# Kernel optimization log

Measured on AMD Instinct MI355X. Metric: run time of the kernel, lower is better.

The kernel has to match this reference:

```python
import jax, jax.numpy as jnp
import numpy as np

N_QUBITS = 4
N_LAYERS = 2
BN_EPS = 1e-5


def _bcast(t, ref):
    t = jnp.asarray(t)
    return t.reshape(t.shape + (1,) * (ref.ndim - t.ndim))


def apply_ry(state, theta, wire):
    # state: [B, 2,2,2,2] complex; theta: scalar or [B]
    ax = wire + 1
    s0 = jnp.take(state, 0, axis=ax)
    s1 = jnp.take(state, 1, axis=ax)
    half = jnp.asarray(theta, jnp.float32) * 0.5
    c = _bcast(jnp.cos(half), s0)
    s = _bcast(jnp.sin(half), s0)
    return jnp.stack([c * s0 - s * s1, s * s0 + c * s1], axis=ax)


def apply_rz(state, theta, wire):
    ax = wire + 1
    s0 = jnp.take(state, 0, axis=ax)
    s1 = jnp.take(state, 1, axis=ax)
    half = jnp.asarray(theta, jnp.float32) * 0.5
    p = _bcast(jnp.exp(-1j * half), s0)  # complex64
    return jnp.stack([p * s0, jnp.conj(p) * s1], axis=ax)


def apply_cnot(state, control, target):
    ca, ta = control + 1, target + 1
    c0 = jnp.take(state, 0, axis=ca)
    c1 = jnp.take(state, 1, axis=ca)
    ta2 = ta - 1 if ta > ca else ta  # axis shift after take
    c1 = jnp.flip(c1, axis=ta2)      # X on target within control=1 block
    return jnp.stack([c0, c1], axis=ca)


def quantum_layer(x_q_in, qw):
    # Faithful to QuantumLayer.forward: extra tanh on (already tanh'd) input.
    B = x_q_in.shape[0]
    ang = jnp.tanh(x_q_in) * jnp.float32(np.pi)  # [B, n_qubits]
    state = jnp.zeros((B, 2 ** N_QUBITS), jnp.complex64).at[:, 0].set(1.0)
    state = state.reshape((B,) + (2,) * N_QUBITS)
    for i in range(N_QUBITS):
        state = apply_ry(state, ang[:, i], i)
    for l in range(N_LAYERS):
        for i in range(N_QUBITS):
            state = apply_ry(state, qw[l, i, 0], i)
            state = apply_rz(state, qw[l, i, 1], i)
        for i in range(N_QUBITS):
            state = apply_cnot(state, i, (i + 1) % N_QUBITS)
    probs = state.real ** 2 + state.imag ** 2  # [B,2,2,2,2]
    zs = []
    for i in range(N_QUBITS):
        d = jnp.take(probs, 0, axis=i + 1) - jnp.take(probs, 1, axis=i + 1)
        zs.append(jnp.sum(d, axis=tuple(range(1, d.ndim))))
    return jnp.stack(zs, axis=1).astype(jnp.float32)  # [B, n_qubits]


def forward(x, W1, b1, bn_g, bn_b, bn_m, bn_v, W2, b2, qw, W3, b3):
    # pre_quantum (eval mode: dropouts are identity)
    h = jax.nn.relu(x @ W1.T + b1)                       # [B,64]
    h = (h - bn_m) * jax.lax.rsqrt(bn_v + BN_EPS) * bn_g + bn_b
    xq = jnp.tanh(h @ W2.T + b2)                          # [B,4]
    q = quantum_layer(xq, qw)                             # [B,4]
    return q @ W3.T + b3                                  # [B,num_classes]


def setup_inputs() -> dict:
    key = jax.random.key(0)
    ks = jax.random.split(key, 8)
    B, D, H, Q, C = 32768, 1280, 64, N_QUBITS, 10
    return {
        "x": jax.random.normal(ks[0], (B, D), jnp.float32),
        "W1": jax.random.normal(ks[1], (H, D), jnp.float32) * 0.02,
        "b1": jnp.zeros((H,), jnp.float32),
        "bn_g": jnp.ones((H,), jnp.float32),
        "bn_b": jnp.zeros((H,), jnp.float32),
        "bn_m": jnp.zeros((H,), jnp.float32),
        "bn_v": jnp.ones((H,), jnp.float32),
        "W2": jax.random.normal(ks[2], (Q, H), jnp.float32) * 0.1,
        "b2": jnp.zeros((Q,), jnp.float32),
        "qw": jax.random.normal(ks[3], (N_LAYERS, Q, 2), jnp.float32) * 0.1,
        "W3": jax.random.normal(ks[4], (C, Q), jnp.float32) * 0.1,
        "b3": jnp.zeros((C,), jnp.float32),
    }


def reference(x, W1, b1, bn_g, bn_b, bn_m, bn_v, W2, b2, qw, W3, b3):
    return forward(x, W1, b1, bn_g, bn_b, bn_m, bn_v, W2, b2, qw, W3, b3)
```

## Files before the change

kernel.cpp:

```cpp
#include <hip/hip_runtime.h>
#include <math.h>

typedef __attribute__((ext_vector_type(8))) short bf16x8;
typedef __attribute__((ext_vector_type(4))) float f32x4;

constexpr int D   = 1280;
constexpr int H   = 64;
constexpr int BM  = 64;
constexpr int KC  = 64;
constexpr int SW  = KC + 8;
constexpr int HSS = H + 1;

union FragU { bf16x8 v; unsigned int u[4]; };

__device__ __forceinline__ unsigned int pack_split(float f0, float f1, unsigned int& lo) {
    unsigned int u0 = __float_as_uint(f0), u1 = __float_as_uint(f1);
    unsigned int h0 = u0 & 0xFFFF0000u,    h1 = u1 & 0xFFFF0000u;
    float l0 = f0 - __uint_as_float(h0);
    float l1 = f1 - __uint_as_float(h1);
    lo = (__float_as_uint(l1) & 0xFFFF0000u) | (__float_as_uint(l0) >> 16);
    return h1 | (u0 >> 16);
}

template<int BW>
__device__ __forceinline__ void ry_gate(float re[16], float im[16], float theta) {
    float sn, cs;
    sincosf(0.5f * theta, &sn, &cs);
#pragma unroll
    for (int s0 = 0; s0 < 16; ++s0) {
        if (s0 & BW) continue;
        const int s1 = s0 | BW;
        float r0 = re[s0], i0 = im[s0], r1 = re[s1], i1 = im[s1];
        re[s0] = cs * r0 - sn * r1;  im[s0] = cs * i0 - sn * i1;
        re[s1] = sn * r0 + cs * r1;  im[s1] = sn * i0 + cs * i1;
    }
}

template<int BW>
__device__ __forceinline__ void rz_gate(float re[16], float im[16], float theta) {
    float sn, cs;
    sincosf(0.5f * theta, &sn, &cs);
#pragma unroll
    for (int s0 = 0; s0 < 16; ++s0) {
        if (s0 & BW) continue;
        const int s1 = s0 | BW;
        float r0 = re[s0], i0 = im[s0], r1 = re[s1], i1 = im[s1];
        re[s0] = cs * r0 + sn * i0;  im[s0] = cs * i0 - sn * r0;
        re[s1] = cs * r1 - sn * i1;  im[s1] = cs * i1 + sn * r1;
    }
}

template<int BWC, int BWT>
__device__ __forceinline__ void cnot_gate(float re[16], float im[16]) {
#pragma unroll
    for (int s = 0; s < 16; ++s) {
        if (!(s & BWC)) continue;
        if (s & BWT) continue;
        const int t = s | BWT;
        float tr = re[s], ti = im[s];
        re[s] = re[t]; im[s] = im[t];
        re[t] = tr;    im[t] = ti;
    }
}

__global__ __launch_bounds__(256, 2)
void fused_qh_mfma(const float* __restrict__ x,   const float* __restrict__ W1,
                   const float* __restrict__ b1,  const float* __restrict__ bn_g,
                   const float* __restrict__ bn_b,const float* __restrict__ bn_m,
                   const float* __restrict__ bn_v,const float* __restrict__ W2,
                   const float* __restrict__ b2,  const float* __restrict__ qw,
                   const float* __restrict__ W3,  const float* __restrict__ b3,
                   float* __restrict__ out)
{
    __shared__ short whi[H][SW];
    __shared__ short wlo[H][SW];
    __shared__ float hs[BM][HSS];
    __shared__ float w2s[4 * H];
    __shared__ float b1s[H], scl[H], shf[H];

    const int tid  = threadIdx.x;
    const int l    = tid & 63;
    const int w    = tid >> 6;
    const int lr   = l & 15;
    const int lk   = l >> 4;
    const int row0 = blockIdx.x * BM;

    w2s[tid] = W2[tid];
    if (tid < H) {
        float s = bn_g[tid] * rsqrtf(bn_v[tid] + 1e-5f);
        b1s[tid] = b1[tid];
        scl[tid] = s;
        shf[tid] = bn_b[tid] - bn_m[tid] * s;
    }

    const float4* xr4 = reinterpret_cast<const float4*>(x + (size_t)(row0 + w * 16 + lr) * D);

    int sn[4], sk4[4];
#pragma unroll
    for (int it = 0; it < 4; ++it) {
        int f4 = tid + it * 256;
        sn[it]  = f4 >> 4;
        sk4[it] = (f4 & 15) * 4;
    }

    f32x4 acc[4] = {{0,0,0,0},{0,0,0,0},{0,0,0,0},{0,0,0,0}};

    float4 acur[4], anxt[4], wcur[4], wnxt[4];
#pragma unroll
    for (int it = 0; it < 4; ++it)
        wcur[it] = *reinterpret_cast<const float4*>(&W1[(size_t)sn[it] * D + sk4[it]]);
#pragma unroll
    for (int h = 0; h < 2; ++h)
#pragma unroll
        for (int p = 0; p < 2; ++p)
            acur[h * 2 + p] = xr4[h * 8 + lk * 2 + p];

    for (int k0 = 0; k0 < D; k0 += KC) {
#pragma unroll
        for (int it = 0; it < 4; ++it) {
            unsigned int lo01, lo23;
            unsigned int hi01 = pack_split(wcur[it].x, wcur[it].y, lo01);
            unsigned int hi23 = pack_split(wcur[it].z, wcur[it].w, lo23);
            uint2 hv; hv.x = hi01; hv.y = hi23;
            uint2 lv; lv.x = lo01; lv.y = lo23;
            *reinterpret_cast<uint2*>(&whi[sn[it]][sk4[it]]) = hv;
            *reinterpret_cast<uint2*>(&wlo[sn[it]][sk4[it]]) = lv;
        }
        if (k0 + KC < D) {
            const int kn = k0 + KC;
#pragma unroll
            for (int it = 0; it < 4; ++it)
                wnxt[it] = *reinterpret_cast<const float4*>(&W1[(size_t)sn[it] * D + kn + sk4[it]]);
#pragma unroll
            for (int h = 0; h < 2; ++h)
#pragma unroll
                for (int p = 0; p < 2; ++p)
                    anxt[h * 2 + p] = xr4[kn / 4 + h * 8 + lk * 2 + p];
        }
        __syncthreads();

        FragU ahi[2], alo[2];
#pragma unroll
        for (int h = 0; h < 2; ++h) {
            const float4 a0 = acur[h * 2 + 0];
            const float4 a1 = acur[h * 2 + 1];
            ahi[h].u[0] = pack_split(a0.x, a0.y, alo[h].u[0]);
            ahi[h].u[1] = pack_split(a0.z, a0.w, alo[h].u[1]);
            ahi[h].u[2] = pack_split(a1.x, a1.y, alo[h].u[2]);
            ahi[h].u[3] = pack_split(a1.z, a1.w, alo[h].u[3]);
        }

#pragma unroll
        for (int h = 0; h < 2; ++h) {
#pragma unroll
            for (int g = 0; g < 4; ++g) {
                const bf16x8 bh = *reinterpret_cast<const bf16x8*>(&whi[g * 16 + lr][h * 32 + lk * 8]);
                const bf16x8 bl = *reinterpret_cast<const bf16x8*>(&wlo[g * 16 + lr][h * 32 + lk * 8]);
                acc[g] = __builtin_amdgcn_mfma_f32_16x16x32_bf16(ahi[h].v, bh, acc[g], 0, 0, 0);
                acc[g] = __builtin_amdgcn_mfma_f32_16x16x32_bf16(ahi[h].v, bl, acc[g], 0, 0, 0);
                acc[g] = __builtin_amdgcn_mfma_f32_16x16x32_bf16(alo[h].v, bh, acc[g], 0, 0, 0);
            }
        }
        __syncthreads();

#pragma unroll
        for (int it = 0; it < 4; ++it) { acur[it] = anxt[it]; wcur[it] = wnxt[it]; }
    }

#pragma unroll
    for (int g = 0; g < 4; ++g) {
        const int c = g * 16 + lr;
        const float b1c = b1s[c], s = scl[c], sh = shf[c];
#pragma unroll
        for (int r = 0; r < 4; ++r) {
            float v = acc[g][r] + b1c;
            v = fmaxf(v, 0.0f) * s + sh;
            hs[w * 16 + lk * 4 + r][c] = v;
        }
    }
    __syncthreads();

    if (tid < BM) {
        const int row = tid;

        float ang[4];
#pragma unroll
        for (int qi = 0; qi < 4; ++qi) {
            float a2 = b2[qi];
            for (int k = 0; k < H; ++k)
                a2 = fmaf(hs[row][k], w2s[qi * H + k], a2);
            float xq = tanhf(a2);
            ang[qi] = tanhf(xq) * 3.14159265358979323846f;
        }

        float re[16] = {}, im[16] = {};
        re[0] = 1.0f;
        ry_gate<8>(re, im, ang[0]);
        ry_gate<4>(re, im, ang[1]);
        ry_gate<2>(re, im, ang[2]);
        ry_gate<1>(re, im, ang[3]);

#pragma unroll
        for (int ll = 0; ll < 2; ++ll) {
            const float* qp = &qw[ll * 8];
            ry_gate<8>(re, im, qp[0]); rz_gate<8>(re, im, qp[1]);
            ry_gate<4>(re, im, qp[2]); rz_gate<4>(re, im, qp[3]);
            ry_gate<2>(re, im, qp[4]); rz_gate<2>(re, im, qp[5]);
            ry_gate<1>(re, im, qp[6]); rz_gate<1>(re, im, qp[7]);
            cnot_gate<8, 4>(re, im);
            cnot_gate<4, 2>(re, im);
            cnot_gate<2, 1>(re, im);
            cnot_gate<1, 8>(re, im);
        }

        float z[4] = {};
#pragma unroll
        for (int s = 0; s < 16; ++s) {
            float p = re[s] * re[s] + im[s] * im[s];
            z[0] += (s & 8) ? -p : p;
            z[1] += (s & 4) ? -p : p;
            z[2] += (s & 2) ? -p : p;
            z[3] += (s & 1) ? -p : p;
        }

        float* o = &out[(size_t)(row0 + row) * 10];
#pragma unroll
        for (int c = 0; c < 10; ++c) {
            float v = b3[c];
#pragma unroll
            for (int i = 0; i < 4; ++i)
                v = fmaf(z[i], W3[c * 4 + i], v);
            o[c] = v;
        }
    }
}

extern "C" void kernel_launch(void* const* d_in, const int* in_sizes, int n_in,
                              void* d_out, int out_size, void* d_ws, size_t ws_size,
                              hipStream_t stream) {
    const float* x    = (const float*)d_in[0];
    const float* W1   = (const float*)d_in[1];
    const float* b1   = (const float*)d_in[2];
    const float* bn_g = (const float*)d_in[3];
    const float* bn_b = (const float*)d_in[4];
    const float* bn_m = (const float*)d_in[5];
    const float* bn_v = (const float*)d_in[6];
    const float* W2   = (const float*)d_in[7];
    const float* b2   = (const float*)d_in[8];
    const float* qw   = (const float*)d_in[9];
    const float* W3   = (const float*)d_in[10];
    const float* b3   = (const float*)d_in[11];
    float* out = (float*)d_out;

    const int B = in_sizes[0] / D;
    const int grid = B / BM;

    fused_qh_mfma<<<grid, 256, 0, stream>>>(
        x, W1, b1, bn_g, bn_b, bn_m, bn_v, W2, b2, qw, W3, b3, out);
}
```

Measured before the change: 43.69 us.

## Pre-split W1 into MFMA fragment layout in workspace and drop LDS staging

Adds a pre-pass kernel that splits W1 into bf16 hi/lo parts, stored in MFMA fragment order in the workspace. The main kernel then reads B fragments straight from global memory (L2-resident), with no LDS tile staging and no per-chunk barriers. It also double-buffers x loads across chunk pairs and spreads the W2 projection across all 256 threads instead of 64. The cost is an extra kernel launch, plus every block re-reading W1 fragments from cache. It falls back to the old kernel if the workspace is too small.

```diff
diff --git a/kernel.cpp b/kernel.cpp
--- a/kernel.cpp
+++ b/kernel.cpp
@@ -8,7 +8,8 @@
 constexpr int H   = 64;
 constexpr int BM  = 64;
 constexpr int KC  = 64;
-constexpr int SW  = KC + 8;
+constexpr int NCH = D / KC;
+constexpr int WFRAG_ELEMS = (D / 32) * 4 * 64 * 8;
 constexpr int HSS = H + 1;
 
 union FragU { bf16x8 v; unsigned int u[4]; };
@@ -62,6 +63,192 @@
         re[t] = tr;    im[t] = ti;
     }
 }
+
+__device__ __forceinline__ void quantum_row(const float ang[4], const float* __restrict__ qw,
+                                            const float* __restrict__ W3, const float* __restrict__ b3,
+                                            float* __restrict__ o) {
+    float re[16] = {}, im[16] = {};
+    re[0] = 1.0f;
+    ry_gate<8>(re, im, ang[0]);
+    ry_gate<4>(re, im, ang[1]);
+    ry_gate<2>(re, im, ang[2]);
+    ry_gate<1>(re, im, ang[3]);
+#pragma unroll
+    for (int ll = 0; ll < 2; ++ll) {
+        const float* qp = &qw[ll * 8];
+        ry_gate<8>(re, im, qp[0]); rz_gate<8>(re, im, qp[1]);
+        ry_gate<4>(re, im, qp[2]); rz_gate<4>(re, im, qp[3]);
+        ry_gate<2>(re, im, qp[4]); rz_gate<2>(re, im, qp[5]);
+        ry_gate<1>(re, im, qp[6]); rz_gate<1>(re, im, qp[7]);
+        cnot_gate<8, 4>(re, im);
+        cnot_gate<4, 2>(re, im);
+        cnot_gate<2, 1>(re, im);
+        cnot_gate<1, 8>(re, im);
+    }
+    float z[4] = {};
+#pragma unroll
+    for (int s = 0; s < 16; ++s) {
+        float p = re[s] * re[s] + im[s] * im[s];
+        z[0] += (s & 8) ? -p : p;
+        z[1] += (s & 4) ? -p : p;
+        z[2] += (s & 2) ? -p : p;
+        z[3] += (s & 1) ? -p : p;
+    }
+#pragma unroll
+    for (int c = 0; c < 10; ++c) {
+        float v = b3[c];
+#pragma unroll
+        for (int i = 0; i < 4; ++i)
+            v = fmaf(z[i], W3[c * 4 + i], v);
+        o[c] = v;
+    }
+}
+
+__global__ __launch_bounds__(256)
+void convert_w1(const float* __restrict__ W1, short* __restrict__ whi, short* __restrict__ wlo) {
+    const int t  = blockIdx.x * 256 + threadIdx.x;
+    const int kh = t >> 8;
+    const int g  = (t >> 6) & 3;
+    const int l  = t & 63;
+    const int n  = g * 16 + (l & 15);
+    const int k  = kh * 32 + (l >> 4) * 8;
+    const float4* p = reinterpret_cast<const float4*>(&W1[(size_t)n * D + k]);
+    const float4 a = p[0], b = p[1];
+    FragU hi, lo;
+    hi.u[0] = pack_split(a.x, a.y, lo.u[0]);
+    hi.u[1] = pack_split(a.z, a.w, lo.u[1]);
+    hi.u[2] = pack_split(b.x, b.y, lo.u[2]);
+    hi.u[3] = pack_split(b.z, b.w, lo.u[3]);
+    *reinterpret_cast<bf16x8*>(&whi[(size_t)t * 8]) = hi.v;
+    *reinterpret_cast<bf16x8*>(&wlo[(size_t)t * 8]) = lo.v;
+}
+
+__device__ __forceinline__ void do_chunk(int c, const float4 (&buf)[4],
+                                         const bf16x8* __restrict__ WH,
+                                         const bf16x8* __restrict__ WL,
+                                         int l, f32x4 (&acc)[4]) {
+    bf16x8 bh[2][4], bl[2][4];
+#pragma unroll
+    for (int h = 0; h < 2; ++h)
+#pragma unroll
+        for (int g = 0; g < 4; ++g) {
+            const int idx = ((c * 2 + h) * 4 + g) * 64 + l;
+            bh[h][g] = WH[idx];
+            bl[h][g] = WL[idx];
+        }
+    FragU ahi[2], alo[2];
+#pragma unroll
+    for (int h = 0; h < 2; ++h) {
+        const float4 a0 = buf[h * 2 + 0];
+        const float4 a1 = buf[h * 2 + 1];
+        ahi[h].u[0] = pack_split(a0.x, a0.y, alo[h].u[0]);
+        ahi[h].u[1] = pack_split(a0.z, a0.w, alo[h].u[1]);
+        ahi[h].u[2] = pack_split(a1.x, a1.y, alo[h].u[2]);
+        ahi[h].u[3] = pack_split(a1.z, a1.w, alo[h].u[3]);
+    }
+#pragma unroll
+    for (int h = 0; h < 2; ++h)
+#pragma unroll
+        for (int g = 0; g < 4; ++g) {
+            acc[g] = __builtin_amdgcn_mfma_f32_16x16x32_bf16(ahi[h].v, bh[h][g], acc[g], 0, 0, 0);
+            acc[g] = __builtin_amdgcn_mfma_f32_16x16x32_bf16(ahi[h].v, bl[h][g], acc[g], 0, 0, 0);
+            acc[g] = __builtin_amdgcn_mfma_f32_16x16x32_bf16(alo[h].v, bh[h][g], acc[g], 0, 0, 0);
+        }
+}
+
+__global__ __launch_bounds__(256, 2)
+void fused_qh_nolds(const float* __restrict__ x,   const short* __restrict__ whi_g,
+                    const short* __restrict__ wlo_g,
+                    const float* __restrict__ b1,  const float* __restrict__ bn_g,
+                    const float* __restrict__ bn_b,const float* __restrict__ bn_m,
+                    const float* __restrict__ bn_v,const float* __restrict__ W2,
+                    const float* __restrict__ b2,  const float* __restrict__ qw,
+                    const float* __restrict__ W3,  const float* __restrict__ b3,
+                    float* __restrict__ out)
+{
+    __shared__ float hs[BM][HSS];
+    __shared__ float angs[BM][4];
+    __shared__ float w2s[4 * H];
+    __shared__ float b1s[H], scl[H], shf[H];
+
+    const int tid  = threadIdx.x;
+    const int l    = tid & 63;
+    const int w    = tid >> 6;
+    const int lr   = l & 15;
+    const int lk   = l >> 4;
+    const int row0 = blockIdx.x * BM;
+
+    w2s[tid] = W2[tid];
+    if (tid < H) {
+        float s = bn_g[tid] * rsqrtf(bn_v[tid] + 1e-5f);
+        b1s[tid] = b1[tid];
+        scl[tid] = s;
+        shf[tid] = bn_b[tid] - bn_m[tid] * s;
+    }
+    __syncthreads();
+
+    const float4* xr4 = reinterpret_cast<const float4*>(x + (size_t)(row0 + w * 16 + lr) * D);
+    const bf16x8* WH  = reinterpret_cast<const bf16x8*>(whi_g);
+    const bf16x8* WL  = reinterpret_cast<const bf16x8*>(wlo_g);
+
+    f32x4 acc[4] = {{0,0,0,0},{0,0,0,0},{0,0,0,0},{0,0,0,0}};
+
+#define LOADX(dst, c)                                                  \
+    {                                                                  \
+        _Pragma("unroll")                                              \
+        for (int i = 0; i < 4; ++i)                                    \
+            dst[i] = xr4[(c) * 16 + (i >> 1) * 8 + lk * 2 + (i & 1)];  \
+    }
+
+    float4 bA[4], bB[4], nA[4], nB[4];
+    LOADX(bA, 0);
+    LOADX(bB, 1);
+
+#pragma unroll
+    for (int cc = 0; cc < NCH / 2; ++cc) {
+        const int c0 = 2 * cc, c1 = 2 * cc + 1;
+        if (c0 + 2 < NCH) LOADX(nA, c0 + 2);
+        do_chunk(c0, bA, WH, WL, l, acc);
+#pragma unroll
+        for (int i = 0; i < 4; ++i) bA[i] = nA[i];
+        if (c1 + 2 < NCH) LOADX(nB, c1 + 2);
+        do_chunk(c1, bB, WH, WL, l, acc);
+#pragma unroll
+        for (int i = 0; i < 4; ++i) bB[i] = nB[i];
+    }
+#undef LOADX
+
+#pragma unroll
+    for (int g = 0; g < 4; ++g) {
+        const int c = g * 16 + lr;
+        const float b1c = b1s[c], s = scl[c], sh = shf[c];
+#pragma unroll
+        for (int r = 0; r < 4; ++r) {
+            float v = acc[g][r] + b1c;
+            v = fmaxf(v, 0.0f) * s + sh;
+            hs[w * 16 + lk * 4 + r][c] = v;
+        }
+    }
+    __syncthreads();
+
+    {
+        const int row = tid >> 2, qi = tid & 3;
+        float a2 = b2[qi];
+#pragma unroll
+        for (int k = 0; k < H; ++k)
+            a2 = fmaf(hs[row][k], w2s[qi * H + k], a2);
+        float xq = tanhf(a2);
+        angs[row][qi] = tanhf(xq) * 3.14159265358979323846f;
+    }
+    __syncthreads();
+
+    if (tid < BM) {
+        float ang[4] = { angs[tid][0], angs[tid][1], angs[tid][2], angs[tid][3] };
+        quantum_row(ang, qw, W3, b3, &out[(size_t)(row0 + tid) * 10]);
+    }
+}
+
+constexpr int SW = KC + 8;
 
 __global__ __launch_bounds__(256, 2)
 void fused_qh_mfma(const float* __restrict__ x,   const float* __restrict__ W1,
@@ -104,7 +291,6 @@
     }
 
     f32x4 acc[4] = {{0,0,0,0},{0,0,0,0},{0,0,0,0},{0,0,0,0}};
-
     float4 acur[4], anxt[4], wcur[4], wnxt[4];
 #pragma unroll
     for (int it = 0; it < 4; ++it)
@@ -149,9 +335,8 @@
             ahi[h].u[2] = pack_split(a1.x, a1.y, alo[h].u[2]);
             ahi[h].u[3] = pack_split(a1.z, a1.w, alo[h].u[3]);
         }
-
-#pragma unroll
-        for (int h = 0; h < 2; ++h) {
+#pragma unroll
+        for (int h = 0; h < 2; ++h)
 #pragma unroll
             for (int g = 0; g < 4; ++g) {
                 const bf16x8 bh = *reinterpret_cast<const bf16x8*>(&whi[g * 16 + lr][h * 32 + lk * 8]);
@@ -160,7 +345,6 @@
                 acc[g] = __builtin_amdgcn_mfma_f32_16x16x32_bf16(ahi[h].v, bl, acc[g], 0, 0, 0);
                 acc[g] = __builtin_amdgcn_mfma_f32_16x16x32_bf16(alo[h].v, bh, acc[g], 0, 0, 0);
             }
-        }
         __syncthreads();
 
 #pragma unroll
@@ -182,7 +366,6 @@
 
     if (tid < BM) {
         const int row = tid;
-
         float ang[4];
 #pragma unroll
         for (int qi = 0; qi < 4; ++qi) {
@@ -192,46 +375,7 @@
             float xq = tanhf(a2);
             ang[qi] = tanhf(xq) * 3.14159265358979323846f;
         }
-
-        float re[16] = {}, im[16] = {};
-        re[0] = 1.0f;
-        ry_gate<8>(re, im, ang[0]);
-        ry_gate<4>(re, im, ang[1]);
-        ry_gate<2>(re, im, ang[2]);
-        ry_gate<1>(re, im, ang[3]);
-
-#pragma unroll
-        for (int ll = 0; ll < 2; ++ll) {
-            const float* qp = &qw[ll * 8];
-            ry_gate<8>(re, im, qp[0]); rz_gate<8>(re, im, qp[1]);
-            ry_gate<4>(re, im, qp[2]); rz_gate<4>(re, im, qp[3]);
-            ry_gate<2>(re, im, qp[4]); rz_gate<2>(re, im, qp[5]);
-            ry_gate<1>(re, im, qp[6]); rz_gate<1>(re, im, qp[7]);
-            cnot_gate<8, 4>(re, im);
-            cnot_gate<4, 2>(re, im);
-            cnot_gate<2, 1>(re, im);
-            cnot_gate<1, 8>(re, im);
-        }
-
-        float z[4] = {};
-#pragma unroll
-        for (int s = 0; s < 16; ++s) {
-            float p = re[s] * re[s] + im[s] * im[s];
-            z[0] += (s & 8) ? -p : p;
-            z[1] += (s & 4) ? -p : p;
-            z[2] += (s & 2) ? -p : p;
-            z[3] += (s & 1) ? -p : p;
-        }
-
-        float* o = &out[(size_t)(row0 + row) * 10];
-#pragma unroll
-        for (int c = 0; c < 10; ++c) {
-            float v = b3[c];
-#pragma unroll
-            for (int i = 0; i < 4; ++i)
-                v = fmaf(z[i], W3[c * 4 + i], v);
-            o[c] = v;
-        }
+        quantum_row(ang, qw, W3, b3, &out[(size_t)(row0 + row) * 10]);
     }
 }
 
@@ -255,6 +399,15 @@
     const int B = in_sizes[0] / D;
     const int grid = B / BM;
 
-    fused_qh_mfma<<<grid, 256, 0, stream>>>(
-        x, W1, b1, bn_g, bn_b, bn_m, bn_v, W2, b2, qw, W3, b3, out);
-}
+    const size_t need = (size_t)2 * WFRAG_ELEMS * sizeof(short);
+    if (ws_size >= need) {
+        short* whi_ws = (short*)d_ws;
+        short* wlo_ws = whi_ws + WFRAG_ELEMS;
+        convert_w1<<<(WFRAG_ELEMS / 8) / 256, 256, 0, stream>>>(W1, whi_ws, wlo_ws);
+        fused_qh_nolds<<<grid, 256, 0, stream>>>(
+            x, whi_ws, wlo_ws, b1, bn_g, bn_b, bn_m, bn_v, W2, b2, qw, W3, b3, out);
+    } else {
+        fused_qh_mfma<<<grid, 256, 0, stream>>>(
+            x, W1, b1, bn_g, bn_b, bn_m, bn_v, W2, b2, qw, W3, b3, out);
+    }
+}
```

Result: slower. 62.12 us (+42.2%).

## Halve row tile, split waves over M and N, parallelize W2 projection

Applied to the files above, without the earlier changes.

Reduces rows per block from 64 to 32, so each of the 4 waves now computes a 16x32 output tile (2 wave rows by 2 column halves) instead of 16x64. This doubles the grid and raises launch_bounds occupancy to 4 blocks per CU. The W2 projection is now spread across 4 threads per row through a shared angle buffer rather than being done serially by one thread. The trade-off is that each block still converts and stages the full W1 tile while covering half as many rows, which doubles per-row W1 staging and split work.

```diff
diff --git a/kernel.cpp b/kernel.cpp
--- a/kernel.cpp
+++ b/kernel.cpp
@@ -6,7 +6,7 @@
 
 constexpr int D   = 1280;
 constexpr int H   = 64;
-constexpr int BM  = 64;
+constexpr int BM  = 32;
 constexpr int KC  = 64;
 constexpr int SW  = KC + 8;
 constexpr int HSS = H + 1;
@@ -63,24 +63,67 @@
     }
 }
 
-__global__ __launch_bounds__(256, 2)
-void fused_qh_mfma(const float* __restrict__ x,   const float* __restrict__ W1,
-                   const float* __restrict__ b1,  const float* __restrict__ bn_g,
-                   const float* __restrict__ bn_b,const float* __restrict__ bn_m,
-                   const float* __restrict__ bn_v,const float* __restrict__ W2,
-                   const float* __restrict__ b2,  const float* __restrict__ qw,
-                   const float* __restrict__ W3,  const float* __restrict__ b3,
-                   float* __restrict__ out)
+__device__ __forceinline__ void quantum_row(const float ang[4], const float* __restrict__ qw,
+                                            const float* __restrict__ W3, const float* __restrict__ b3,
+                                            float* __restrict__ o) {
+    float re[16] = {}, im[16] = {};
+    re[0] = 1.0f;
+    ry_gate<8>(re, im, ang[0]);
+    ry_gate<4>(re, im, ang[1]);
+    ry_gate<2>(re, im, ang[2]);
+    ry_gate<1>(re, im, ang[3]);
+#pragma unroll
+    for (int ll = 0; ll < 2; ++ll) {
+        const float* qp = &qw[ll * 8];
+        ry_gate<8>(re, im, qp[0]); rz_gate<8>(re, im, qp[1]);
+        ry_gate<4>(re, im, qp[2]); rz_gate<4>(re, im, qp[3]);
+        ry_gate<2>(re, im, qp[4]); rz_gate<2>(re, im, qp[5]);
+        ry_gate<1>(re, im, qp[6]); rz_gate<1>(re, im, qp[7]);
+        cnot_gate<8, 4>(re, im);
+        cnot_gate<4, 2>(re, im);
+        cnot_gate<2, 1>(re, im);
+        cnot_gate<1, 8>(re, im);
+    }
+    float z[4] = {};
+#pragma unroll
+    for (int s = 0; s < 16; ++s) {
+        float p = re[s] * re[s] + im[s] * im[s];
+        z[0] += (s & 8) ? -p : p;
+        z[1] += (s & 4) ? -p : p;
+        z[2] += (s & 2) ? -p : p;
+        z[3] += (s & 1) ? -p : p;
+    }
+#pragma unroll
+    for (int c = 0; c < 10; ++c) {
+        float v = b3[c];
+#pragma unroll
+        for (int i = 0; i < 4; ++i)
+            v = fmaf(z[i], W3[c * 4 + i], v);
+        o[c] = v;
+    }
+}
+
+__global__ __launch_bounds__(256, 4)
+void fused_qh_v8(const float* __restrict__ x,   const float* __restrict__ W1,
+                 const float* __restrict__ b1,  const float* __restrict__ bn_g,
+                 const float* __restrict__ bn_b,const float* __restrict__ bn_m,
+                 const float* __restrict__ bn_v,const float* __restrict__ W2,
+                 const float* __restrict__ b2,  const float* __restrict__ qw,
+                 const float* __restrict__ W3,  const float* __restrict__ b3,
+                 float* __restrict__ out)
 {
     __shared__ short whi[H][SW];
     __shared__ short wlo[H][SW];
     __shared__ float hs[BM][HSS];
     __shared__ float w2s[4 * H];
     __shared__ float b1s[H], scl[H], shf[H];
+    __shared__ float angs[BM][4];
 
     const int tid  = threadIdx.x;
     const int l    = tid & 63;
     const int w    = tid >> 6;
+    const int wm   = w & 1;
+    const int wn   = w >> 1;
     const int lr   = l & 15;
     const int lk   = l >> 4;
     const int row0 = blockIdx.x * BM;
@@ -93,7 +136,7 @@
         shf[tid] = bn_b[tid] - bn_m[tid] * s;
     }
 
-    const float4* xr4 = reinterpret_cast<const float4*>(x + (size_t)(row0 + w * 16 + lr) * D);
+    const float4* xr4 = reinterpret_cast<const float4*>(x + (size_t)(row0 + wm * 16 + lr) * D);
 
     int sn[4], sk4[4];
 #pragma unroll
@@ -103,8 +146,7 @@
         sk4[it] = (f4 & 15) * 4;
     }
 
-    f32x4 acc[4] = {{0,0,0,0},{0,0,0,0},{0,0,0,0},{0,0,0,0}};
-
+    f32x4 acc[2] = {{0,0,0,0},{0,0,0,0}};
     float4 acur[4], anxt[4], wcur[4], wnxt[4];
 #pragma unroll
     for (int it = 0; it < 4; ++it)
@@ -142,25 +184,25 @@
         FragU ahi[2], alo[2];
 #pragma unroll
         for (int h = 0; h < 2; ++h) {
-            const float4 a0 = acur[h * 2 + 0];
-            const float4 a1 = acur[h * 2 + 1];
-            ahi[h].u[0] = pack_split(a0.x, a0.y, alo[h].u[0]);
-            ahi[h].u[1] = pack_split(a0.z, a0.w, alo[h].u[1]);
-            ahi[h].u[2] = pack_split(a1.x, a1.y, alo[h].u[2]);
-            ahi[h].u[3] = pack_split(a1.z, a1.w, alo[h].u[3]);
-        }
-
-#pragma unroll
-        for (int h = 0; h < 2; ++h) {
-#pragma unroll
-            for (int g = 0; g < 4; ++g) {
+            const float4 p0 = acur[h * 2 + 0];
+            const float4 p1 = acur[h * 2 + 1];
+            ahi[h].u[0] = pack_split(p0.x, p0.y, alo[h].u[0]);
+            ahi[h].u[1] = pack_split(p0.z, p0.w, alo[h].u[1]);
+            ahi[h].u[2] = pack_split(p1.x, p1.y, alo[h].u[2]);
+            ahi[h].u[3] = pack_split(p1.z, p1.w, alo[h].u[3]);
+        }
+
+#pragma unroll
+        for (int h = 0; h < 2; ++h)
+#pragma unroll
+            for (int g2 = 0; g2 < 2; ++g2) {
+                const int g = wn * 2 + g2;
                 const bf16x8 bh = *reinterpret_cast<const bf16x8*>(&whi[g * 16 + lr][h * 32 + lk * 8]);
                 const bf16x8 bl = *reinterpret_cast<const bf16x8*>(&wlo[g * 16 + lr][h * 32 + lk * 8]);
-                acc[g] = __builtin_amdgcn_mfma_f32_16x16x32_bf16(ahi[h].v, bh, acc[g], 0, 0, 0);
-                acc[g] = __builtin_amdgcn_mfma_f32_16x16x32_bf16(ahi[h].v, bl, acc[g], 0, 0, 0);
-                acc[g] = __builtin_amdgcn_mfma_f32_16x16x32_bf16(alo[h].v, bh, acc[g], 0, 0, 0);
+                acc[g2] = __builtin_amdgcn_mfma_f32_16x16x32_bf16(ahi[h].v, bh, acc[g2], 0, 0, 0);
+                acc[g2] = __builtin_amdgcn_mfma_f32_16x16x32_bf16(ahi[h].v, bl, acc[g2], 0, 0, 0);
+                acc[g2] = __builtin_amdgcn_mfma_f32_16x16x32_bf16(alo[h].v, bh, acc[g2], 0, 0, 0);
             }
-        }
         __syncthreads();
 
 #pragma unroll
@@ -168,70 +210,32 @@
     }
 
 #pragma unroll
-    for (int g = 0; g < 4; ++g) {
-        const int c = g * 16 + lr;
-        const float b1c = b1s[c], s = scl[c], sh = shf[c];
+    for (int g2 = 0; g2 < 2; ++g2) {
+        const int cc = (wn * 2 + g2) * 16 + lr;
+        const float b1c = b1s[cc], s = scl[cc], sh = shf[cc];
 #pragma unroll
         for (int r = 0; r < 4; ++r) {
-            float v = acc[g][r] + b1c;
+            float v = acc[g2][r] + b1c;
             v = fmaxf(v, 0.0f) * s + sh;
-            hs[w * 16 + lk * 4 + r][c] = v;
+            hs[wm * 16 + lk * 4 + r][cc] = v;
         }
     }
     __syncthreads();
 
+    if (tid < 4 * BM) {
+        const int row = tid >> 2, qi = tid & 3;
+        float a2v = b2[qi];
+#pragma unroll
+        for (int k = 0; k < H; ++k)
+            a2v = fmaf(hs[row][k], w2s[qi * H + k], a2v);
+        float xq = tanhf(a2v);
+        angs[row][qi] = tanhf(xq) * 3.14159265358979323846f;
+    }
+    __syncthreads();
+
     if (tid < BM) {
-        const int row = tid;
-
-        float ang[4];
-#pragma unroll
-        for (int qi = 0; qi < 4; ++qi) {
-            float a2 = b2[qi];
-            for (int k = 0; k < H; ++k)
-                a2 = fmaf(hs[row][k], w2s[qi * H + k], a2);
-            float xq = tanhf(a2);
-            ang[qi] = tanhf(xq) * 3.14159265358979323846f;
-        }
-
-        float re[16] = {}, im[16] = {};
-        re[0] = 1.0f;
-        ry_gate<8>(re, im, ang[0]);
-        ry_gate<4>(re, im, ang[1]);
-        ry_gate<2>(re, im, ang[2]);
-        ry_gate<1>(re, im, ang[3]);
-
-#pragma unroll
-        for (int ll = 0; ll < 2; ++ll) {
-            const float* qp = &qw[ll * 8];
-            ry_gate<8>(re, im, qp[0]); rz_gate<8>(re, im, qp[1]);
-            ry_gate<4>(re, im, qp[2]); rz_gate<4>(re, im, qp[3]);
-            ry_gate<2>(re, im, qp[4]); rz_gate<2>(re, im, qp[5]);
-            ry_gate<1>(re, im, qp[6]); rz_gate<1>(re, im, qp[7]);
-            cnot_gate<8, 4>(re, im);
-            cnot_gate<4, 2>(re, im);
-            cnot_gate<2, 1>(re, im);
-            cnot_gate<1, 8>(re, im);
-        }
-
-        float z[4] = {};
-#pragma unroll
-        for (int s = 0; s < 16; ++s) {
-            float p = re[s] * re[s] + im[s] * im[s];
-            z[0] += (s & 8) ? -p : p;
-            z[1] += (s & 4) ? -p : p;
-            z[2] += (s & 2) ? -p : p;
-            z[3] += (s & 1) ? -p : p;
-        }
-
-        float* o = &out[(size_t)(row0 + row) * 10];
-#pragma unroll
-        for (int c = 0; c < 10; ++c) {
-            float v = b3[c];
-#pragma unroll
-            for (int i = 0; i < 4; ++i)
-                v = fmaf(z[i], W3[c * 4 + i], v);
-            o[c] = v;
-        }
+        float ang[4] = { angs[tid][0], angs[tid][1], angs[tid][2], angs[tid][3] };
+        quantum_row(ang, qw, W3, b3, &out[(size_t)(row0 + tid) * 10]);
     }
 }
 
@@ -255,6 +259,6 @@
     const int B = in_sizes[0] / D;
     const int grid = B / BM;
 
-    fused_qh_mfma<<<grid, 256, 0, stream>>>(
+    fused_qh_v8<<<grid, 256, 0, stream>>>(
         x, W1, b1, bn_g, bn_b, bn_m, bn_v, W2, b2, qw, W3, b3, out);
 }
```

Measured after the change: 71.17 us. +62.9%, slower.
